# Performance work log

Measured on AMD Instinct MI355X. Metric: run time of the kernel, lower is better.

Reference implementation:

```python
import jax, jax.numpy as jnp
import numpy as np

N = 199968   # active voxels (flat tokens)
W = 3125     # number of windows
S = 64       # window capacity
D = 128      # d_model
H = 8        # nhead
DH = D // H
DFF = 256


def layer_norm(x, g, b, eps=1e-5):
    m = x.mean(-1, keepdims=True)
    v = ((x - m) ** 2).mean(-1, keepdims=True)
    return (x - m) / jnp.sqrt(v + eps) * g + b


def setup_inputs() -> dict:
    key = jax.random.key(0)
    ks = jax.random.split(key, 12)
    s = 0.02
    src = jax.random.normal(ks[0], (N, D), dtype=jnp.float32)
    pos = jax.random.normal(ks[1], (W, S, D), dtype=jnp.float32)
    # token i occupies flat window-slot i; slots >= N are padding
    inds = jnp.arange(N, dtype=jnp.int64)
    key_padding_mask = (jnp.arange(W * S) >= N).reshape(W, S)  # True = pad
    in_proj_w = jax.random.normal(ks[2], (3 * D, D), dtype=jnp.float32) * s
    in_proj_b = jax.random.normal(ks[3], (3 * D,), dtype=jnp.float32) * s
    out_w = jax.random.normal(ks[4], (D, D), dtype=jnp.float32) * s
    out_b = jax.random.normal(ks[5], (D,), dtype=jnp.float32) * s
    w1 = jax.random.normal(ks[6], (DFF, D), dtype=jnp.float32) * s
    b1 = jax.random.normal(ks[7], (DFF,), dtype=jnp.float32) * s
    w2 = jax.random.normal(ks[8], (D, DFF), dtype=jnp.float32) * s
    b2 = jax.random.normal(ks[9], (D,), dtype=jnp.float32) * s
    ln1_g = jnp.ones((D,), jnp.float32); ln1_b = jnp.zeros((D,), jnp.float32)
    ln2_g = jnp.ones((D,), jnp.float32); ln2_b = jnp.zeros((D,), jnp.float32)
    return {"src": src, "pos": pos, "inds": inds,
            "key_padding_mask": key_padding_mask,
            "in_proj_w": in_proj_w, "in_proj_b": in_proj_b,
            "out_w": out_w, "out_b": out_b,
            "w1": w1, "b1": b1, "w2": w2, "b2": b2,
            "ln1_g": ln1_g, "ln1_b": ln1_b, "ln2_g": ln2_g, "ln2_b": ln2_b}


def reference(src, pos, inds, key_padding_mask, in_proj_w, in_proj_b,
              out_w, out_b, w1, b1, w2, b2, ln1_g, ln1_b, ln2_g, ln2_b):
    # ---- flat2window_v2: scatter flat tokens into window slots ----
    win = jnp.zeros((W * S, D), src.dtype).at[inds].set(src).reshape(W, S, D)
    # q = k = feat + pos, v = feat (post-norm, self-attention branch)
    qk_in = win + pos
    Wq, Wk, Wv = in_proj_w[:D], in_proj_w[D:2 * D], in_proj_w[2 * D:]
    bq, bk, bv = in_proj_b[:D], in_proj_b[D:2 * D], in_proj_b[2 * D:]
    q = (qk_in @ Wq.T + bq).reshape(W, S, H, DH)
    k = (qk_in @ Wk.T + bk).reshape(W, S, H, DH)
    v = (win @ Wv.T + bv).reshape(W, S, H, DH)
    scale = 1.0 / jnp.sqrt(jnp.asarray(DH, src.dtype))
    scores = jnp.einsum('wqhd,wkhd->whqk', q, k) * scale  # [W,H,S,S]
    scores = jnp.where(key_padding_mask[:, None, None, :], -jnp.inf, scores)
    attn = jax.nn.softmax(scores, axis=-1)
    o = jnp.einsum('whqk,wkhd->wqhd', attn, v).reshape(W, S, D)
    o = o @ out_w.T + out_b
    # ---- window2flat_v2: gather back to flat tokens ----
    att_out = o.reshape(W * S, D)[inds]
    # ---- residual + LN + FFN + LN (post_norm=True, dropout=0 eval) ----
    x = layer_norm(src + att_out, ln1_g, ln1_b)
    ffn = jax.nn.relu(x @ w1.T + b1) @ w2.T + b2
    x = layer_norm(x + ffn, ln2_g, ln2_b)
    return x
```

## Files before the change

### kernel.cpp

```cpp
#include <hip/hip_runtime.h>
#include <stdint.h>

typedef __attribute__((ext_vector_type(8))) short bf16x8;
typedef __attribute__((ext_vector_type(4))) float f32x4;
typedef __attribute__((ext_vector_type(16))) float f32x16;

#define MFMA16(a,b,c) __builtin_amdgcn_mfma_f32_16x16x32_bf16((a),(b),(c),0,0,0)
#define MFMA32(a,b,c) __builtin_amdgcn_mfma_f32_32x32x16_bf16((a),(b),(c),0,0,0)

#define RA 0
#define RB 16384
#define RC 32768
#define RED 49152
#define LDSB (49152 + 2048)
#define QSCALE 0.36067376022224085f

static __device__ __forceinline__ int swz16(int row, int byte){ return byte ^ ((row&15)<<4); }
static __device__ __forceinline__ int swz8 (int row, int byte){ return byte ^ ((row&7)<<4); }

static __device__ __forceinline__ uint32_t cvtpk(float lo, float hi){
  uint32_t r; asm("v_cvt_pk_bf16_f32 %0, %1, %2" : "=v"(r) : "v"(lo), "v"(hi)); return r;
}
static __device__ __forceinline__ unsigned short f2bf(float f){
  union { float f; uint32_t u; } c; c.f = f;
  return (unsigned short)((c.u + 0x7fffu + ((c.u >> 16) & 1u)) >> 16);
}
static __device__ __forceinline__ f32x16 zero16(){
  f32x16 z;
  #pragma unroll
  for (int e=0;e<16;++e) z[e]=0.f;
  return z;
}

static __device__ __forceinline__ void packPT(const f32x16 s, int hi, bf16x8& fA, bf16x8& fB){
  uint32_t PA0=cvtpk(s[0],s[1]),  PA1=cvtpk(s[2],s[3]);
  uint32_t PB0=cvtpk(s[4],s[5]),  PB1=cvtpk(s[6],s[7]);
  uint32_t PC0=cvtpk(s[8],s[9]),  PC1=cvtpk(s[10],s[11]);
  uint32_t PD0=cvtpk(s[12],s[13]),PD1=cvtpk(s[14],s[15]);
  uint32_t x0 = __shfl_xor(hi ? PA0 : PB0, 32);
  uint32_t x1 = __shfl_xor(hi ? PA1 : PB1, 32);
  uint32_t y0 = __shfl_xor(hi ? PC0 : PD0, 32);
  uint32_t y1 = __shfl_xor(hi ? PC1 : PD1, 32);
  union { uint32_t u[4]; bf16x8 v; } ua, ub;
  ua.u[0] = hi ? x0 : PA0;  ua.u[1] = hi ? x1 : PA1;
  ua.u[2] = hi ? PB0 : x0;  ua.u[3] = hi ? PB1 : x1;
  ub.u[0] = hi ? y0 : PC0;  ub.u[1] = hi ? y1 : PC1;
  ub.u[2] = hi ? PD0 : y0;  ub.u[3] = hi ? PD1 : y1;
  fA = ua.v; fB = ub.v;
}

__global__ void convert_weights(const float* __restrict__ ipw, const float* __restrict__ ow,
                                const float* __restrict__ w1, const float* __restrict__ w2,
                                unsigned short* __restrict__ wsb){
  int i = blockIdx.x*256 + threadIdx.x;
  if (i >= 131072) return;
  const float* sp; int m, K, KC;
  if (i < 49152)      { sp = ipw; m = i;         K=128; KC=4; }
  else if (i < 65536) { sp = ow;  m = i - 49152; K=128; KC=4; }
  else if (i < 98304) { sp = w1;  m = i - 65536; K=128; KC=4; }
  else                { sp = w2;  m = i - 98304; K=256; KC=8; }
  int e  = m & 7;
  int L  = (m >> 3) & 63;
  int b  = m >> 9;
  int kc = b % KC;
  int Mt = b / KC;
  float v = sp[(Mt*16 + (L&15))*K + kc*32 + (L>>4)*8 + e];
  if (i < 16384) v *= QSCALE;
  wsb[i] = f2bf(v);
}

__global__ __launch_bounds__(256, 3) void enc_kernel(
    const float* __restrict__ src, const float* __restrict__ pos,
    const float* __restrict__ ipb, const float* __restrict__ obp,
    const float* __restrict__ b1p, const float* __restrict__ b2p,
    const float* __restrict__ g1p, const float* __restrict__ be1p,
    const float* __restrict__ g2p, const float* __restrict__ be2p,
    const unsigned short* __restrict__ wb,
    float* __restrict__ out, int nTok)
{
  __shared__ __align__(16) char sm[LDSB];
  const int win  = blockIdx.x;
  const int tid  = threadIdx.x;
  const int lane = tid & 63;
  const int wid  = tid >> 6;
  const int l15  = lane & 15;
  const int lg   = lane >> 4;
  const int l31  = lane & 31;
  const int hi   = lane >> 5;
  const f32x4 FZ = {0.f,0.f,0.f,0.f};
  const int colbase = wid*32;
  const unsigned short* wlane = wb + lane*8;
  const int valid = nTok - win*64;

  f32x4 srcv[2][4];
  #pragma unroll
  for (int Mtl=0;Mtl<2;++Mtl){
    #pragma unroll
    for (int g=0;g<4;++g){
      int row  = g*16 + l15;
      int grow = win*64 + row;
      int col  = colbase + Mtl*16 + lg*4;
      f32x4 sv = FZ;
      if (grow < nTok) sv = *(const f32x4*)(src + (size_t)grow*128 + col);
      f32x4 pv = *(const f32x4*)(pos + (size_t)win*8192 + row*128 + col);
      srcv[Mtl][g] = sv;
      uint2 wv, qv;
      wv.x = cvtpk(sv[0], sv[1]);             wv.y = cvtpk(sv[2], sv[3]);
      qv.x = cvtpk(sv[0]+pv[0], sv[1]+pv[1]); qv.y = cvtpk(sv[2]+pv[2], sv[3]+pv[3]);
      int cb = col*2;
      *(uint2*)(sm + RA + row*256 + swz16(row, cb)) = qv;
      *(uint2*)(sm + RB + row*256 + swz16(row, cb)) = wv;
    }
  }
  __syncthreads();

  {
    {
      bf16x8 wv8[8];
      #pragma unroll
      for (int i=0;i<8;++i)
        wv8[i] = *(const bf16x8*)(wlane + (size_t)(((16 + wid*2 + (i>>2))*4 + (i&3)) << 9));
      f32x4 vacc[2][4];
      #pragma unroll
      for (int Mtl=0;Mtl<2;++Mtl){
        #pragma unroll
        for (int g=0;g<4;++g) vacc[Mtl][g] = FZ;
      }
      #pragma unroll
      for (int kc=0;kc<4;++kc){
        bf16x8 bw[4];
        #pragma unroll
        for (int g=0;g<4;++g){
          int r2 = g*16 + l15;
          bw[g] = *(const bf16x8*)(sm + RB + r2*256 + swz16(r2, kc*64 + lg*16));
        }
        #pragma unroll
        for (int Mtl=0;Mtl<2;++Mtl){
          #pragma unroll
          for (int g=0;g<4;++g) vacc[Mtl][g] = MFMA16(wv8[Mtl*4+kc], bw[g], vacc[Mtl][g]);
        }
      }
      #pragma unroll
      for (int Mtl=0;Mtl<2;++Mtl){
        f32x4 b4 = *(const f32x4*)(ipb + 256 + colbase + Mtl*16 + lg*4);
        #pragma unroll
        for (int g=0;g<4;++g){
          #pragma unroll
          for (int r=0;r<4;++r){
            int d = colbase + Mtl*16 + lg*4 + r, tok = g*16 + l15;
            *(unsigned short*)(sm + RC + d*128 + swz8(d, tok*2)) = f2bf(vacc[Mtl][g][r] + b4[r]);
          }
        }
      }
    }

    f32x4 qacc[2][4];
    {
      bf16x8 wq8[8];
      #pragma unroll
      for (int i=0;i<8;++i)
        wq8[i] = *(const bf16x8*)(wlane + (size_t)((( 0 + wid*2 + (i>>2))*4 + (i&3)) << 9));
      #pragma unroll
      for (int Mtl=0;Mtl<2;++Mtl){
        #pragma unroll
        for (int g=0;g<4;++g) qacc[Mtl][g]=FZ;
      }
      #pragma unroll
      for (int kc=0;kc<4;++kc){
        bf16x8 bq[4];
        #pragma unroll
        for (int g=0;g<4;++g){
          int r2 = g*16 + l15;
          bq[g] = *(const bf16x8*)(sm + RA + r2*256 + swz16(r2, kc*64 + lg*16));
        }
        #pragma unroll
        for (int Mtl=0;Mtl<2;++Mtl){
          #pragma unroll
          for (int g=0;g<4;++g) qacc[Mtl][g] = MFMA16(wq8[Mtl*4+kc], bq[g], qacc[Mtl][g]);
        }
      }
    }
    __syncthreads();

    #pragma unroll
    for (int Mtl=0;Mtl<2;++Mtl){
      f32x4 qb4 = *(const f32x4*)(ipb + colbase + Mtl*16 + lg*4);
      #pragma unroll
      for (int g=0;g<4;++g){
        int tok = g*16 + l15;
        int cb  = (colbase + Mtl*16 + lg*4)*2;
        *(uint32_t*)(sm + RB + tok*256 + swz16(tok, cb))     = cvtpk(qacc[Mtl][g][0]+qb4[0]*QSCALE, qacc[Mtl][g][1]+qb4[1]*QSCALE);
        *(uint32_t*)(sm + RB + tok*256 + swz16(tok, cb + 4)) = cvtpk(qacc[Mtl][g][2]+qb4[2]*QSCALE, qacc[Mtl][g][3]+qb4[3]*QSCALE);
      }
    }

    f32x4 kacc[2][4];
    {
      bf16x8 wk8[8];
      #pragma unroll
      for (int i=0;i<8;++i)
        wk8[i] = *(const bf16x8*)(wlane + (size_t)((( 8 + wid*2 + (i>>2))*4 + (i&3)) << 9));
      #pragma unroll
      for (int Mtl=0;Mtl<2;++Mtl){
        #pragma unroll
        for (int g=0;g<4;++g) kacc[Mtl][g]=FZ;
      }
      #pragma unroll
      for (int kc=0;kc<4;++kc){
        bf16x8 bq[4];
        #pragma unroll
        for (int g=0;g<4;++g){
          int r2 = g*16 + l15;
          bq[g] = *(const bf16x8*)(sm + RA + r2*256 + swz16(r2, kc*64 + lg*16));
        }
        #pragma unroll
        for (int Mtl=0;Mtl<2;++Mtl){
          #pragma unroll
          for (int g=0;g<4;++g) kacc[Mtl][g] = MFMA16(wk8[Mtl*4+kc], bq[g], kacc[Mtl][g]);
        }
      }
    }
    __syncthreads();

    #pragma unroll
    for (int Mtl=0;Mtl<2;++Mtl){
      f32x4 kb4 = *(const f32x4*)(ipb + 128 + colbase + Mtl*16 + lg*4);
      #pragma unroll
      for (int g=0;g<4;++g){
        int tok = g*16 + l15;
        int cb  = (colbase + Mtl*16 + lg*4)*2;
        *(uint32_t*)(sm + RA + tok*256 + swz16(tok, cb))     = cvtpk(kacc[Mtl][g][0]+kb4[0], kacc[Mtl][g][1]+kb4[1]);
        *(uint32_t*)(sm + RA + tok*256 + swz16(tok, cb + 4)) = cvtpk(kacc[Mtl][g][2]+kb4[2], kacc[Mtl][g][3]+kb4[3]);
      }
    }
  }

  #pragma unroll
  for (int hh=0; hh<2; ++hh){
    const int head = wid*2 + hh;
    bf16x8 ka0 = *(const bf16x8*)(sm + RA + (     l31)*256 + swz16(l31,    head*32 + hi*16));
    bf16x8 ka1 = *(const bf16x8*)(sm + RA + (32 + l31)*256 + swz16(32+l31, head*32 + hi*16));
    #pragma unroll
    for (int qt=0; qt<2; ++qt){
      int qrow = qt*32 + l31;
      bf16x8 qb = *(const bf16x8*)(sm + RB + qrow*256 + swz16(qrow, head*32 + hi*16));
      f32x16 s0 = MFMA32(ka0, qb, zero16());
      f32x16 s1 = MFMA32(ka1, qb, zero16());
      if (valid < 64){
        #pragma unroll
        for (int e=0;e<16;++e){
          int kk = (e&3) + 8*(e>>2) + 4*hi;
          if (kk      >= valid) s0[e] = -1e30f;
          if (kk + 32 >= valid) s1[e] = -1e30f;
        }
      }
      #pragma unroll
      for (int e=0;e<16;++e) s0[e] = __builtin_amdgcn_exp2f(s0[e]);
      #pragma unroll
      for (int e=0;e<16;++e) s1[e] = __builtin_amdgcn_exp2f(s1[e]);
      float t[8];
      #pragma unroll
      for (int e=0;e<8;++e) t[e] = (s0[2*e]+s0[2*e+1]) + (s1[2*e]+s1[2*e+1]);
      float u0 = t[0]+t[1], u1 = t[2]+t[3], u2 = t[4]+t[5], u3 = t[6]+t[7];
      float sum = (u0+u1)+(u2+u3);
      sum += __shfl_xor(sum, 32);
      float rden = __builtin_amdgcn_rcpf(sum);

      bf16x8 fr[4];
      packPT(s0, hi, fr[0], fr[1]);
      packPT(s1, hi, fr[2], fr[3]);
      f32x16 oacc = zero16();
      #pragma unroll
      for (int kc=0;kc<4;++kc){
        int vrow = head*16 + l15;
        bf16x8 va = *(const bf16x8*)(sm + RC + vrow*128 + swz8(vrow, kc*32 + hi*16));
        oacc = MFMA32(va, fr[kc], oacc);
      }
      int tok = qt*32 + l31;
      uint32_t q0 = cvtpk(oacc[0]*rden, oacc[1]*rden);
      uint32_t q1 = cvtpk(oacc[2]*rden, oacc[3]*rden);
      uint32_t q2 = cvtpk(oacc[4]*rden, oacc[5]*rden);
      uint32_t q3 = cvtpk(oacc[6]*rden, oacc[7]*rden);
      *(uint32_t*)(sm + RB + tok*256 + swz16(tok, (head*16 + 4*hi    )*2)) = q0;
      *(uint32_t*)(sm + RB + tok*256 + swz16(tok, (head*16 + 4*hi + 2)*2)) = q1;
      *(uint32_t*)(sm + RB + tok*256 + swz16(tok, (head*16 + 8 + 4*hi    )*2)) = q2;
      *(uint32_t*)(sm + RB + tok*256 + swz16(tok, (head*16 + 8 + 4*hi + 2)*2)) = q3;
    }
  }
  __syncthreads();

  f32x4 xva[2][4];
  {
    bf16x8 wo8[8];
    #pragma unroll
    for (int i=0;i<8;++i)
      wo8[i] = *(const bf16x8*)(wlane + 49152 + (size_t)(((wid*2 + (i>>2))*4 + (i&3)) << 9));
    f32x4 oa[2][4];
    #pragma unroll
    for (int Mtl=0;Mtl<2;++Mtl){
      #pragma unroll
      for (int g=0;g<4;++g) oa[Mtl][g] = FZ;
    }
    #pragma unroll
    for (int kc=0;kc<4;++kc){
      bf16x8 bo[4];
      #pragma unroll
      for (int g=0;g<4;++g){
        int r2 = g*16 + l15;
        bo[g] = *(const bf16x8*)(sm + RB + r2*256 + swz16(r2, kc*64 + lg*16));
      }
      #pragma unroll
      for (int Mtl=0;Mtl<2;++Mtl){
        #pragma unroll
        for (int g=0;g<4;++g) oa[Mtl][g] = MFMA16(wo8[Mtl*4+kc], bo[g], oa[Mtl][g]);
      }
    }
    #pragma unroll
    for (int Mtl=0;Mtl<2;++Mtl){
      f32x4 ob4 = *(const f32x4*)(obp + colbase + Mtl*16 + lg*4);
      #pragma unroll
      for (int g=0;g<4;++g){
        #pragma unroll
        for (int r=0;r<4;++r) xva[Mtl][g][r] = oa[Mtl][g][r] + ob4[r] + srcv[Mtl][g][r];
      }
    }
    float* redc = (float*)(sm + RED);
    #pragma unroll
    for (int g=0;g<4;++g){
      float ts=0.f, tq=0.f;
      #pragma unroll
      for (int Mtl=0;Mtl<2;++Mtl){
        #pragma unroll
        for (int r=0;r<4;++r){ float v = xva[Mtl][g][r]; ts += v; tq += v*v; }
      }
      ts += __shfl_xor(ts,16); tq += __shfl_xor(tq,16);
      ts += __shfl_xor(ts,32); tq += __shfl_xor(tq,32);
      if (lg == 0) *(float2*)(redc + (g*16+l15)*8 + wid*2) = make_float2(ts, tq);
    }
    __syncthreads();
    float mean4[4], rstd4[4];
    #pragma unroll
    for (int g=0;g<4;++g){
      int tok = g*16 + l15;
      f32x4 ra = *(const f32x4*)(redc + tok*8);
      f32x4 rb = *(const f32x4*)(redc + tok*8 + 4);
      float sum = ra[0]+ra[2]+rb[0]+rb[2];
      float sq  = ra[1]+ra[3]+rb[1]+rb[3];
      mean4[g] = sum*(1.f/128.f);
      rstd4[g] = __builtin_amdgcn_rsqf(sq*(1.f/128.f) - mean4[g]*mean4[g] + 1e-5f);
    }
    #pragma unroll
    for (int Mtl=0;Mtl<2;++Mtl){
      f32x4 g4 = *(const f32x4*)(g1p  + colbase + Mtl*16 + lg*4);
      f32x4 e4 = *(const f32x4*)(be1p + colbase + Mtl*16 + lg*4);
      #pragma unroll
      for (int g=0;g<4;++g){
        int tok = g*16 + l15;
        int cb  = (colbase + Mtl*16 + lg*4)*2;
        #pragma unroll
        for (int r=0;r<4;++r) xva[Mtl][g][r] = (xva[Mtl][g][r]-mean4[g])*rstd4[g]*g4[r] + e4[r];
        *(uint32_t*)(sm + RA + tok*256 + swz16(tok, cb))     = cvtpk(xva[Mtl][g][0], xva[Mtl][g][1]);
        *(uint32_t*)(sm + RA + tok*256 + swz16(tok, cb + 4)) = cvtpk(xva[Mtl][g][2], xva[Mtl][g][3]);
      }
    }
  }
  __syncthreads();

  {
    char* hreg = (wid < 2) ? (sm + RB) : (sm + RC);
    int   hoff = (wid & 1)*64;
    #pragma unroll 1
    for (int half=0; half<2; ++half){
      bf16x8 wf[8];
      #pragma unroll
      for (int i=0;i<8;++i)
        wf[i] = *(const bf16x8*)(wlane + 65536 + (size_t)(((wid*4 + half*2 + (i>>2))*4 + (i&3)) << 9));
      f32x4 ha[2][4];
      #pragma unroll
      for (int Mtl=0;Mtl<2;++Mtl){
        #pragma unroll
        for (int g=0;g<4;++g) ha[Mtl][g] = FZ;
      }
      #pragma unroll
      for (int kc=0;kc<4;++kc){
        bf16x8 bx[4];
        #pragma unroll
        for (int g=0;g<4;++g){
          int r2 = g*16 + l15;
          bx[g] = *(const bf16x8*)(sm + RA + r2*256 + swz16(r2, kc*64 + lg*16));
        }
        #pragma unroll
        for (int Mtl=0;Mtl<2;++Mtl){
          #pragma unroll
          for (int g=0;g<4;++g) ha[Mtl][g] = MFMA16(wf[Mtl*4+kc], bx[g], ha[Mtl][g]);
        }
      }
      #pragma unroll
      for (int Mtl=0;Mtl<2;++Mtl){
        int Mg = half*2 + Mtl;
        f32x4 b14 = *(const f32x4*)(b1p + wid*64 + Mg*16 + lg*4);
        #pragma unroll
        for (int g=0;g<4;++g){
          int tok = g*16 + l15;
          float h0 = fmaxf(ha[Mtl][g][0]+b14[0], 0.f);
          float h1 = fmaxf(ha[Mtl][g][1]+b14[1], 0.f);
          float h2 = fmaxf(ha[Mtl][g][2]+b14[2], 0.f);
          float h3 = fmaxf(ha[Mtl][g][3]+b14[3], 0.f);
          int cb = (hoff + Mg*16 + lg*4)*2;
          *(uint32_t*)(hreg + tok*256 + swz16(tok, cb))     = cvtpk(h0, h1);
          *(uint32_t*)(hreg + tok*256 + swz16(tok, cb + 4)) = cvtpk(h2, h3);
        }
      }
    }
  }
  __syncthreads();

  {
    f32x4 fa[2][4];
    #pragma unroll
    for (int Mtl=0;Mtl<2;++Mtl){
      #pragma unroll
      for (int g=0;g<4;++g) fa[Mtl][g] = FZ;
    }
    #pragma unroll 1
    for (int half=0; half<2; ++half){
      bf16x8 wg[8];
      #pragma unroll
      for (int i=0;i<8;++i)
        wg[i] = *(const bf16x8*)(wlane + 98304 + (size_t)(((wid*2 + (i>>2))*8 + half*4 + (i&3)) << 9));
      const char* hsrc = sm + (half ? RC : RB);
      #pragma unroll
      for (int kc=0;kc<4;++kc){
        bf16x8 bh[4];
        #pragma unroll
        for (int g=0;g<4;++g){
          int r2 = g*16 + l15;
          bh[g] = *(const bf16x8*)(hsrc + r2*256 + swz16(r2, kc*64 + lg*16));
        }
        #pragma unroll
        for (int Mtl=0;Mtl<2;++Mtl){
          #pragma unroll
          for (int g=0;g<4;++g) fa[Mtl][g] = MFMA16(wg[Mtl*4+kc], bh[g], fa[Mtl][g]);
        }
      }
    }
    #pragma unroll
    for (int Mtl=0;Mtl<2;++Mtl){
      f32x4 b24 = *(const f32x4*)(b2p + colbase + Mtl*16 + lg*4);
      #pragma unroll
      for (int g=0;g<4;++g){
        #pragma unroll
        for (int r=0;r<4;++r) fa[Mtl][g][r] += b24[r] + xva[Mtl][g][r];
      }
    }
    float* redc = (float*)(sm + RED);
    #pragma unroll
    for (int g=0;g<4;++g){
      float ts=0.f, tq=0.f;
      #pragma unroll
      for (int Mtl=0;Mtl<2;++Mtl){
        #pragma unroll
        for (int r=0;r<4;++r){ float v = fa[Mtl][g][r]; ts += v; tq += v*v; }
      }
      ts += __shfl_xor(ts,16); tq += __shfl_xor(tq,16);
      ts += __shfl_xor(ts,32); tq += __shfl_xor(tq,32);
      if (lg == 0) *(float2*)(redc + (g*16+l15)*8 + wid*2) = make_float2(ts, tq);
    }
    __syncthreads();
    float mean4[4], rstd4[4];
    #pragma unroll
    for (int g=0;g<4;++g){
      int tok = g*16 + l15;
      f32x4 ra = *(const f32x4*)(redc + tok*8);
      f32x4 rb = *(const f32x4*)(redc + tok*8 + 4);
      float sum = ra[0]+ra[2]+rb[0]+rb[2];
      float sq  = ra[1]+ra[3]+rb[1]+rb[3];
      mean4[g] = sum*(1.f/128.f);
      rstd4[g] = __builtin_amdgcn_rsqf(sq*(1.f/128.f) - mean4[g]*mean4[g] + 1e-5f);
    }
    #pragma unroll
    for (int Mtl=0;Mtl<2;++Mtl){
      f32x4 g4 = *(const f32x4*)(g2p  + colbase + Mtl*16 + lg*4);
      f32x4 e4 = *(const f32x4*)(be2p + colbase + Mtl*16 + lg*4);
      #pragma unroll
      for (int g=0;g<4;++g){
        int tok = g*16 + l15;
        f32x4 o4;
        #pragma unroll
        for (int r=0;r<4;++r) o4[r] = (fa[Mtl][g][r]-mean4[g])*rstd4[g]*g4[r] + e4[r];
        int X = ((colbase + Mtl*16 + lg*4)*4) ^ (l15<<4);
        *(f32x4*)(sm + ((tok<32)? RA : RB) + (tok&31)*512 + X) = o4;
      }
    }
    __syncthreads();
    #pragma unroll
    for (int j=0;j<8;++j){
      int row  = wid*16 + j*2 + hi;
      int grow = win*64 + row;
      if (grow < nTok){
        int X = (l31*16) ^ ((row&15)<<4);
        f32x4 v = *(const f32x4*)(sm + ((row<32)? RA : RB) + (row&31)*512 + X);
        *(f32x4*)(out + (size_t)grow*128 + l31*4) = v;
      }
    }
  }
}

extern "C" void kernel_launch(void* const* d_in, const int* in_sizes, int n_in,
                              void* d_out, int out_size, void* d_ws, size_t ws_size,
                              hipStream_t stream) {
  const float* src = (const float*)d_in[0];
  const float* pos = (const float*)d_in[1];
  const float* ipw = (const float*)d_in[4];
  const float* ipb = (const float*)d_in[5];
  const float* ow  = (const float*)d_in[6];
  const float* ob  = (const float*)d_in[7];
  const float* w1  = (const float*)d_in[8];
  const float* b1  = (const float*)d_in[9];
  const float* w2  = (const float*)d_in[10];
  const float* b2  = (const float*)d_in[11];
  const float* g1  = (const float*)d_in[12];
  const float* be1 = (const float*)d_in[13];
  const float* g2  = (const float*)d_in[14];
  const float* be2 = (const float*)d_in[15];
  int nTok = in_sizes[0] / 128;
  int nWin = in_sizes[1] / 8192;
  unsigned short* wsb = (unsigned short*)d_ws;

  hipLaunchKernelGGL(convert_weights, dim3(512), dim3(256), 0, stream, ipw, ow, w1, w2, wsb);
  hipLaunchKernelGGL(enc_kernel, dim3(nWin), dim3(256), 0, stream,
                     src, pos, ipb, ob, b1, b2, g1, be1, g2, be2, wsb,
                     (float*)d_out, nTok);
}
```

Baseline: 139.8 us.

## Fold LayerNorm1 affine into FFN1 weights and write un-normalized residual early

Folds the LN1 gamma into W1 and precomputes W1·beta+b1 and W1·gamma in a small auxiliary kernel. The FFN1 input can then be the raw residual written to LDS before the LN statistics barrier, with the normalization applied afterwards as rstd*acc - rstd*mean*rowsum + bias. This removes one block barrier and overlaps the LDS write with the reduction. It also replaces __syncthreads with an LDS-only waitcnt barrier and merges paired 32-bit LDS stores into 64-bit stores. The trade-off is an extra tiny launch, and the mean subtraction now happens after a bf16 matmul of un-centred values, which can lose precision.

```diff
diff --git a/kernel.cpp b/kernel.cpp
--- a/kernel.cpp
+++ b/kernel.cpp
@@ -17,6 +17,12 @@
 
 static __device__ __forceinline__ int swz16(int row, int byte){ return byte ^ ((row&15)<<4); }
 static __device__ __forceinline__ int swz8 (int row, int byte){ return byte ^ ((row&7)<<4); }
+
+static __device__ __forceinline__ void barrier_lds(){
+  asm volatile("s_waitcnt lgkmcnt(0)" ::: "memory");
+  __builtin_amdgcn_s_barrier();
+  __builtin_amdgcn_sched_barrier(0);
+}
 
 static __device__ __forceinline__ uint32_t cvtpk(float lo, float hi){
   uint32_t r; asm("v_cvt_pk_bf16_f32 %0, %1, %2" : "=v"(r) : "v"(lo), "v"(hi)); return r;
@@ -51,28 +57,46 @@
 
 __global__ void convert_weights(const float* __restrict__ ipw, const float* __restrict__ ow,
                                 const float* __restrict__ w1, const float* __restrict__ w2,
+                                const float* __restrict__ g1,
                                 unsigned short* __restrict__ wsb){
   int i = blockIdx.x*256 + threadIdx.x;
   if (i >= 131072) return;
   const float* sp; int m, K, KC;
+  bool isw1 = false;
   if (i < 49152)      { sp = ipw; m = i;         K=128; KC=4; }
   else if (i < 65536) { sp = ow;  m = i - 49152; K=128; KC=4; }
-  else if (i < 98304) { sp = w1;  m = i - 65536; K=128; KC=4; }
+  else if (i < 98304) { sp = w1;  m = i - 65536; K=128; KC=4; isw1 = true; }
   else                { sp = w2;  m = i - 98304; K=256; KC=8; }
   int e  = m & 7;
   int L  = (m >> 3) & 63;
   int b  = m >> 9;
   int kc = b % KC;
   int Mt = b / KC;
-  float v = sp[(Mt*16 + (L&15))*K + kc*32 + (L>>4)*8 + e];
+  int d  = kc*32 + (L>>4)*8 + e;
+  float v = sp[(Mt*16 + (L&15))*K + d];
   if (i < 16384) v *= QSCALE;
+  if (isw1)      v *= g1[d];
   wsb[i] = f2bf(v);
+}
+
+__global__ void convert_aux(const float* __restrict__ w1, const float* __restrict__ b1,
+                            const float* __restrict__ g1, const float* __restrict__ be1,
+                            float* __restrict__ auxp){
+  int f = threadIdx.x;
+  float s_be = 0.f, s_g = 0.f;
+  for (int d=0; d<128; ++d){
+    float w = w1[f*128+d];
+    s_be += w * be1[d];
+    s_g  += w * g1[d];
+  }
+  auxp[f]       = b1[f] + s_be;
+  auxp[256 + f] = s_g;
 }
 
 __global__ __launch_bounds__(256, 3) void enc_kernel(
     const float* __restrict__ src, const float* __restrict__ pos,
     const float* __restrict__ ipb, const float* __restrict__ obp,
-    const float* __restrict__ b1p, const float* __restrict__ b2p,
+    const float* __restrict__ b2p,
     const float* __restrict__ g1p, const float* __restrict__ be1p,
     const float* __restrict__ g2p, const float* __restrict__ be2p,
     const unsigned short* __restrict__ wb,
@@ -90,6 +114,7 @@
   const f32x4 FZ = {0.f,0.f,0.f,0.f};
   const int colbase = wid*32;
   const unsigned short* wlane = wb + lane*8;
+  const float* auxp = (const float*)(wb + 131072);
   const int valid = nTok - win*64;
 
   f32x4 srcv[2][4];
@@ -112,7 +137,7 @@
       *(uint2*)(sm + RB + row*256 + swz16(row, cb)) = wv;
     }
   }
-  __syncthreads();
+  barrier_lds();
 
   {
     {
@@ -180,7 +205,7 @@
         }
       }
     }
-    __syncthreads();
+    barrier_lds();
 
     #pragma unroll
     for (int Mtl=0;Mtl<2;++Mtl){
@@ -189,8 +214,10 @@
       for (int g=0;g<4;++g){
         int tok = g*16 + l15;
         int cb  = (colbase + Mtl*16 + lg*4)*2;
-        *(uint32_t*)(sm + RB + tok*256 + swz16(tok, cb))     = cvtpk(qacc[Mtl][g][0]+qb4[0]*QSCALE, qacc[Mtl][g][1]+qb4[1]*QSCALE);
-        *(uint32_t*)(sm + RB + tok*256 + swz16(tok, cb + 4)) = cvtpk(qacc[Mtl][g][2]+qb4[2]*QSCALE, qacc[Mtl][g][3]+qb4[3]*QSCALE);
+        uint2 qp;
+        qp.x = cvtpk(qacc[Mtl][g][0]+qb4[0]*QSCALE, qacc[Mtl][g][1]+qb4[1]*QSCALE);
+        qp.y = cvtpk(qacc[Mtl][g][2]+qb4[2]*QSCALE, qacc[Mtl][g][3]+qb4[3]*QSCALE);
+        *(uint2*)(sm + RB + tok*256 + swz16(tok, cb)) = qp;
       }
     }
 
@@ -220,7 +247,7 @@
         }
       }
     }
-    __syncthreads();
+    barrier_lds();
 
     #pragma unroll
     for (int Mtl=0;Mtl<2;++Mtl){
@@ -229,8 +256,10 @@
       for (int g=0;g<4;++g){
         int tok = g*16 + l15;
         int cb  = (colbase + Mtl*16 + lg*4)*2;
-        *(uint32_t*)(sm + RA + tok*256 + swz16(tok, cb))     = cvtpk(kacc[Mtl][g][0]+kb4[0], kacc[Mtl][g][1]+kb4[1]);
-        *(uint32_t*)(sm + RA + tok*256 + swz16(tok, cb + 4)) = cvtpk(kacc[Mtl][g][2]+kb4[2], kacc[Mtl][g][3]+kb4[3]);
+        uint2 kp;
+        kp.x = cvtpk(kacc[Mtl][g][0]+kb4[0], kacc[Mtl][g][1]+kb4[1]);
+        kp.y = cvtpk(kacc[Mtl][g][2]+kb4[2], kacc[Mtl][g][3]+kb4[3]);
+        *(uint2*)(sm + RA + tok*256 + swz16(tok, cb)) = kp;
       }
     }
   }
@@ -277,19 +306,19 @@
         oacc = MFMA32(va, fr[kc], oacc);
       }
       int tok = qt*32 + l31;
-      uint32_t q0 = cvtpk(oacc[0]*rden, oacc[1]*rden);
-      uint32_t q1 = cvtpk(oacc[2]*rden, oacc[3]*rden);
-      uint32_t q2 = cvtpk(oacc[4]*rden, oacc[5]*rden);
-      uint32_t q3 = cvtpk(oacc[6]*rden, oacc[7]*rden);
-      *(uint32_t*)(sm + RB + tok*256 + swz16(tok, (head*16 + 4*hi    )*2)) = q0;
-      *(uint32_t*)(sm + RB + tok*256 + swz16(tok, (head*16 + 4*hi + 2)*2)) = q1;
-      *(uint32_t*)(sm + RB + tok*256 + swz16(tok, (head*16 + 8 + 4*hi    )*2)) = q2;
-      *(uint32_t*)(sm + RB + tok*256 + swz16(tok, (head*16 + 8 + 4*hi + 2)*2)) = q3;
-    }
-  }
-  __syncthreads();
+      uint2 o01, o23;
+      o01.x = cvtpk(oacc[0]*rden, oacc[1]*rden);
+      o01.y = cvtpk(oacc[2]*rden, oacc[3]*rden);
+      o23.x = cvtpk(oacc[4]*rden, oacc[5]*rden);
+      o23.y = cvtpk(oacc[6]*rden, oacc[7]*rden);
+      *(uint2*)(sm + RB + tok*256 + swz16(tok, (head*16 + 4*hi)*2))     = o01;
+      *(uint2*)(sm + RB + tok*256 + swz16(tok, (head*16 + 8 + 4*hi)*2)) = o23;
+    }
+  }
+  barrier_lds();
 
   f32x4 xva[2][4];
+  float mean4[4], rstd4[4];
   {
     bf16x8 wo8[8];
     #pragma unroll
@@ -337,8 +366,20 @@
       ts += __shfl_xor(ts,32); tq += __shfl_xor(tq,32);
       if (lg == 0) *(float2*)(redc + (g*16+l15)*8 + wid*2) = make_float2(ts, tq);
     }
-    __syncthreads();
-    float mean4[4], rstd4[4];
+    #pragma unroll
+    for (int Mtl=0;Mtl<2;++Mtl){
+      #pragma unroll
+      for (int g=0;g<4;++g){
+        int tok = g*16 + l15;
+        int cb  = (colbase + Mtl*16 + lg*4)*2;
+        uint2 xp;
+        xp.x = cvtpk(xva[Mtl][g][0], xva[Mtl][g][1]);
+        xp.y = cvtpk(xva[Mtl][g][2], xva[Mtl][g][3]);
+        *(uint2*)(sm + RA + tok*256 + swz16(tok, cb)) = xp;
+      }
+    }
+    barrier_lds();
+
     #pragma unroll
     for (int g=0;g<4;++g){
       int tok = g*16 + l15;
@@ -355,16 +396,11 @@
       f32x4 e4 = *(const f32x4*)(be1p + colbase + Mtl*16 + lg*4);
       #pragma unroll
       for (int g=0;g<4;++g){
-        int tok = g*16 + l15;
-        int cb  = (colbase + Mtl*16 + lg*4)*2;
         #pragma unroll
         for (int r=0;r<4;++r) xva[Mtl][g][r] = (xva[Mtl][g][r]-mean4[g])*rstd4[g]*g4[r] + e4[r];
-        *(uint32_t*)(sm + RA + tok*256 + swz16(tok, cb))     = cvtpk(xva[Mtl][g][0], xva[Mtl][g][1]);
-        *(uint32_t*)(sm + RA + tok*256 + swz16(tok, cb + 4)) = cvtpk(xva[Mtl][g][2], xva[Mtl][g][3]);
-      }
-    }
-  }
-  __syncthreads();
+      }
+    }
+  }
 
   {
     char* hreg = (wid < 2) ? (sm + RB) : (sm + RC);
@@ -398,22 +434,26 @@
       #pragma unroll
       for (int Mtl=0;Mtl<2;++Mtl){
         int Mg = half*2 + Mtl;
-        f32x4 b14 = *(const f32x4*)(b1p + wid*64 + Mg*16 + lg*4);
+        f32x4 b1f4 = *(const f32x4*)(auxp +       wid*64 + Mg*16 + lg*4);
+        f32x4 rs14 = *(const f32x4*)(auxp + 256 + wid*64 + Mg*16 + lg*4);
         #pragma unroll
         for (int g=0;g<4;++g){
           int tok = g*16 + l15;
-          float h0 = fmaxf(ha[Mtl][g][0]+b14[0], 0.f);
-          float h1 = fmaxf(ha[Mtl][g][1]+b14[1], 0.f);
-          float h2 = fmaxf(ha[Mtl][g][2]+b14[2], 0.f);
-          float h3 = fmaxf(ha[Mtl][g][3]+b14[3], 0.f);
+          float rr = rstd4[g], cm = rstd4[g]*mean4[g];
+          float h0 = fmaxf(rr*ha[Mtl][g][0] - cm*rs14[0] + b1f4[0], 0.f);
+          float h1 = fmaxf(rr*ha[Mtl][g][1] - cm*rs14[1] + b1f4[1], 0.f);
+          float h2 = fmaxf(rr*ha[Mtl][g][2] - cm*rs14[2] + b1f4[2], 0.f);
+          float h3 = fmaxf(rr*ha[Mtl][g][3] - cm*rs14[3] + b1f4[3], 0.f);
           int cb = (hoff + Mg*16 + lg*4)*2;
-          *(uint32_t*)(hreg + tok*256 + swz16(tok, cb))     = cvtpk(h0, h1);
-          *(uint32_t*)(hreg + tok*256 + swz16(tok, cb + 4)) = cvtpk(h2, h3);
-        }
-      }
-    }
-  }
-  __syncthreads();
+          uint2 hp;
+          hp.x = cvtpk(h0, h1);
+          hp.y = cvtpk(h2, h3);
+          *(uint2*)(hreg + tok*256 + swz16(tok, cb)) = hp;
+        }
+      }
+    }
+  }
+  barrier_lds();
 
   {
     f32x4 fa[2][4];
@@ -466,8 +506,8 @@
       ts += __shfl_xor(ts,32); tq += __shfl_xor(tq,32);
       if (lg == 0) *(float2*)(redc + (g*16+l15)*8 + wid*2) = make_float2(ts, tq);
     }
-    __syncthreads();
-    float mean4[4], rstd4[4];
+    barrier_lds();
+    float m2[4], r2v[4];
     #pragma unroll
     for (int g=0;g<4;++g){
       int tok = g*16 + l15;
@@ -475,8 +515,8 @@
       f32x4 rb = *(const f32x4*)(redc + tok*8 + 4);
       float sum = ra[0]+ra[2]+rb[0]+rb[2];
       float sq  = ra[1]+ra[3]+rb[1]+rb[3];
-      mean4[g] = sum*(1.f/128.f);
-      rstd4[g] = __builtin_amdgcn_rsqf(sq*(1.f/128.f) - mean4[g]*mean4[g] + 1e-5f);
+      m2[g]  = sum*(1.f/128.f);
+      r2v[g] = __builtin_amdgcn_rsqf(sq*(1.f/128.f) - m2[g]*m2[g] + 1e-5f);
     }
     #pragma unroll
     for (int Mtl=0;Mtl<2;++Mtl){
@@ -487,12 +527,12 @@
         int tok = g*16 + l15;
         f32x4 o4;
         #pragma unroll
-        for (int r=0;r<4;++r) o4[r] = (fa[Mtl][g][r]-mean4[g])*rstd4[g]*g4[r] + e4[r];
+        for (int r=0;r<4;++r) o4[r] = (fa[Mtl][g][r]-m2[g])*r2v[g]*g4[r] + e4[r];
         int X = ((colbase + Mtl*16 + lg*4)*4) ^ (l15<<4);
         *(f32x4*)(sm + ((tok<32)? RA : RB) + (tok&31)*512 + X) = o4;
       }
     }
-    __syncthreads();
+    barrier_lds();
     #pragma unroll
     for (int j=0;j<8;++j){
       int row  = wid*16 + j*2 + hi;
@@ -526,9 +566,11 @@
   int nTok = in_sizes[0] / 128;
   int nWin = in_sizes[1] / 8192;
   unsigned short* wsb = (unsigned short*)d_ws;
-
-  hipLaunchKernelGGL(convert_weights, dim3(512), dim3(256), 0, stream, ipw, ow, w1, w2, wsb);
+  float* auxp = (float*)(wsb + 131072);
+
+  hipLaunchKernelGGL(convert_weights, dim3(512), dim3(256), 0, stream, ipw, ow, w1, w2, g1, wsb);
+  hipLaunchKernelGGL(convert_aux, dim3(1), dim3(256), 0, stream, w1, b1, g1, be1, auxp);
   hipLaunchKernelGGL(enc_kernel, dim3(nWin), dim3(256), 0, stream,
-                     src, pos, ipb, ob, b1, b2, g1, be1, g2, be2, wsb,
+                     src, pos, ipb, ob, b2, g1, be1, g2, be2, wsb,
                      (float*)d_out, nTok);
 }
```

After: 158.6 us. +13.5%, slower.
